# Kernel tuning notes

Measured on AMD Instinct MI355X. Metric: run time of the kernel, lower is better.

## Reference

```python
import jax, jax.numpy as jnp
import numpy as np

B, C, H, W = 4, 512, 64, 64
D = 512  # model_dim


def setup_inputs() -> dict:
    key = jax.random.key(0)
    ks = jax.random.split(key, 9)
    s = 0.02
    return {
        "q": jax.random.normal(ks[0], (B, C, H, W), dtype=jnp.float32),
        "Wq": jax.random.normal(ks[1], (D, C), dtype=jnp.float32) * s,
        "bq": jax.random.normal(ks[2], (D,), dtype=jnp.float32) * s,
        "Wk": jax.random.normal(ks[3], (D, C), dtype=jnp.float32) * s,
        "bk": jax.random.normal(ks[4], (D,), dtype=jnp.float32) * s,
        "Wv": jax.random.normal(ks[5], (D, C), dtype=jnp.float32) * s,
        "bv": jax.random.normal(ks[6], (D,), dtype=jnp.float32) * s,
        "Wo": jax.random.normal(ks[7], (C, D), dtype=jnp.float32) * s,
        "bo": jax.random.normal(ks[8], (C,), dtype=jnp.float32) * s,
    }


def reference(q, Wq, bq, Wk, bk, Wv, bv, Wo, bo):
    b, c, h, w = q.shape
    # 1x1 conv == per-pixel linear over channels; tokens s = h*w
    x = q.reshape(b, c, h * w)                      # (b, c, s)
    Q = jnp.einsum('bcs,dc->bsd', x, Wq) + bq       # (b, s, D)
    K = jnp.einsum('bcs,dc->bsd', x, Wk) + bk
    V = jnp.einsum('bcs,dc->bsd', x, Wv) + bv
    # ScaleAttend: scale = q.shape[-1]^-0.5 = model_dim^-0.5 (heads not split)
    scale = jnp.asarray(Q.shape[-1], Q.dtype) ** -0.5
    sim = jnp.einsum('bsd,btd->bst', Q, K) * scale  # (b, s, s)
    attn = jax.nn.softmax(sim, axis=-1)
    o = jnp.einsum('bst,btd->bsd', attn, V)         # (b, s, D)
    # to_out 1x1 conv: D -> C
    y = jnp.einsum('bsd,cd->bsc', o, Wo) + bo       # (b, s, C)
    return y.transpose(0, 2, 1).reshape(b, c, h, w)
```

## Files before the change

kernel.cpp:

```cpp
#include <hip/hip_runtime.h>
#include <hip/hip_bf16.h>

typedef __hip_bfloat16 bf16;
typedef __attribute__((ext_vector_type(8))) short short8;
typedef __attribute__((ext_vector_type(4))) float floatx4;
typedef __attribute__((ext_vector_type(4))) short shortx4;

static constexpr int BATCH = 4;
static constexpr int CH    = 512;
static constexpr int SEQ   = 4096;
static constexpr int DM    = 512;

__device__ __forceinline__ void gload16(const void* g, void* l) {
  __builtin_amdgcn_global_load_lds(
      (const __attribute__((address_space(1))) unsigned int*)g,
      (__attribute__((address_space(3))) unsigned int*)l,
      16, 0, 0);
}

__global__ __launch_bounds__(256) void cvt_weights(
    const float* __restrict__ w0, const float* __restrict__ w1,
    const float* __restrict__ w2, const float* __restrict__ w3,
    bf16* __restrict__ out) {
  const float* src = (blockIdx.y == 0) ? w0 : (blockIdx.y == 1) ? w1
                   : (blockIdx.y == 2) ? w2 : w3;
  int idx = blockIdx.x * 256 + threadIdx.x;
  out[(long)blockIdx.y * (DM * CH) + idx] = __float2bfloat16(src[idx]);
}

__global__ __launch_bounds__(256) void transpose_cvt(
    const float* __restrict__ x, bf16* __restrict__ xT) {
  __shared__ float tile[64][65];
  const int s0 = blockIdx.x * 64, c0 = blockIdx.y * 64;
  const float* xb = x + (long)blockIdx.z * CH * SEQ;
  bf16* xTb = xT + (long)blockIdx.z * SEQ * CH;
  const int t = threadIdx.x;
  const int sl = t & 63, cq = t >> 6;
  #pragma unroll
  for (int i = 0; i < 16; ++i) {
    int cl = cq * 16 + i;
    tile[cl][sl] = xb[(long)(c0 + cl) * SEQ + s0 + sl];
  }
  __syncthreads();
  const int cl2 = t & 63, sq = t >> 6;
  #pragma unroll
  for (int i = 0; i < 16; ++i) {
    int sl2 = sq * 16 + i;
    xTb[(long)(s0 + sl2) * CH + c0 + cl2] = __float2bfloat16(tile[cl2][sl2]);
  }
}

__global__ __launch_bounds__(512, 2) void gemm_qk(
    const bf16* __restrict__ A, long sAz,
    const bf16* __restrict__ B, long sBz,
    bf16* __restrict__ C, long sCz,
    float scale, int K, int ldc) {
  __shared__ __align__(16) bf16 As[2][256 * 64];
  __shared__ __align__(16) bf16 Bs[2][256 * 64];

  int id = blockIdx.x + gridDim.x * (blockIdx.y + gridDim.y * blockIdx.z);
  int nwg = gridDim.x * gridDim.y * gridDim.z;
  int sid = ((nwg & 7) == 0) ? ((id & 7) * (nwg >> 3) + (id >> 3)) : id;
  const int bx = sid % gridDim.x;
  const int by = (sid / gridDim.x) % gridDim.y;
  const int bz = sid / (gridDim.x * gridDim.y);

  const int tid = threadIdx.x;
  const long lK = K;
  const bf16* Ab = A + (long)bz * sAz + (long)by * 256 * lK;
  const bf16* Bb = B + (long)bz * sBz + (long)bx * 256 * lK;

  const int w = tid >> 6, lane = tid & 63;
  const int wr = w >> 2, wc = w & 3;
  const int l16 = lane & 15, quad = lane >> 4;

  const int srow = tid >> 3;
  const int sp = tid & 7;
  const int slog = (sp ^ (srow & 7)) << 3;

  const int pA0 = (quad ^ (l16 & 7)) << 3;
  const int pA1 = pA0 ^ 32;

  auto stage_half = [&](const bf16* Gb, bf16* Lb, int kt, int h) {
    #pragma unroll
    for (int r = 0; r < 2; ++r) {
      const int row = h * 128 + r * 64 + srow;
      gload16(Gb + (long)kt * 64 + (long)row * lK + slog,
              (char*)Lb + row * 128 + sp * 16);
    }
  };

  floatx4 acc[8][4];
  #pragma unroll
  for (int m = 0; m < 8; ++m)
    #pragma unroll
    for (int n = 0; n < 4; ++n) acc[m][n] = (floatx4)(0.0f);

  const int nk = K >> 6;
  stage_half(Ab, &As[0][0], 0, 0); stage_half(Bb, &Bs[0][0], 0, 0);
  stage_half(Ab, &As[0][0], 0, 1); stage_half(Bb, &Bs[0][0], 0, 1);
  if (nk > 1) { stage_half(Ab, &As[1][0], 1, 0); stage_half(Bb, &Bs[1][0], 1, 0); }
  asm volatile("s_waitcnt vmcnt(4)" ::: "memory");
  __builtin_amdgcn_s_barrier();

  for (int tt = 0; tt < nk; tt += 2) {
    #pragma unroll
    for (int u = 0; u < 2; ++u) {
      const bf16* __restrict__ Al = &As[u][0];
      const bf16* __restrict__ Bl = &Bs[u][0];
      short8 a[2][4], b[2][2][2];
      #pragma unroll
      for (int p = 0; p < 4; ++p) {
        const int rm = p >> 1, cn = p & 1;
        if (cn == 0) {
          #pragma unroll
          for (int kc = 0; kc < 2; ++kc)
            #pragma unroll
            for (int i = 0; i < 4; ++i)
              a[kc][i] = *(const short8*)(
                  Al + (rm * 128 + wr * 64 + i * 16 + l16) * 64
                     + (kc ? pA1 : pA0));
        }
        if (rm == 0) {
          #pragma unroll
          for (int kc = 0; kc < 2; ++kc)
            #pragma unroll
            for (int j = 0; j < 2; ++j)
              b[kc][cn][j] = *(const short8*)(
                  Bl + (cn * 128 + wc * 32 + j * 16 + l16) * 64
                     + (kc ? pA1 : pA0));
        }
        {
          const int g = u * 4 + p;
          const int stile = tt + 1 + ((g + 2) >> 2);
          if (stile < nk) {
            const int sh = (p < 2) ? 1 : 0;
            if (p & 1) stage_half(Bb, &Bs[stile & 1][0], stile, sh);
            else       stage_half(Ab, &As[stile & 1][0], stile, sh);
          }
        }
        __builtin_amdgcn_sched_barrier(0);
        __builtin_amdgcn_s_barrier();
        asm volatile("s_waitcnt lgkmcnt(0)" ::: "memory");
        __builtin_amdgcn_sched_barrier(0);
        __builtin_amdgcn_s_setprio(1);
        #pragma unroll
        for (int kc = 0; kc < 2; ++kc)
          #pragma unroll
          for (int i = 0; i < 4; ++i)
            #pragma unroll
            for (int j = 0; j < 2; ++j)
              acc[rm * 4 + i][cn * 2 + j] =
                  __builtin_amdgcn_mfma_f32_16x16x32_bf16(
                      a[kc][i], b[kc][cn][j], acc[rm * 4 + i][cn * 2 + j],
                      0, 0, 0);
        __builtin_amdgcn_s_setprio(0);
        if (p == 3) {
          if (u == 0) {
            if (tt + 2 < nk) asm volatile("s_waitcnt vmcnt(4)" ::: "memory");
            else             asm volatile("s_waitcnt vmcnt(0)" ::: "memory");
          } else {
            if (tt + 2 < nk) asm volatile("s_waitcnt vmcnt(4)" ::: "memory");
          }
        }
        __builtin_amdgcn_s_barrier();
      }
    }
  }

  bf16* Cb = C + (long)bz * sCz;
  #pragma unroll
  for (int rm = 0; rm < 2; ++rm)
    #pragma unroll
    for (int i = 0; i < 4; ++i) {
      const int row = by * 256 + rm * 128 + wr * 64 + i * 16 + quad * 4;
      #pragma unroll
      for (int cn = 0; cn < 2; ++cn)
        #pragma unroll
        for (int j = 0; j < 2; ++j) {
          const int col = bx * 256 + cn * 128 + wc * 32 + j * 16 + l16;
          floatx4 v = acc[rm * 4 + i][cn * 2 + j];
          #pragma unroll
          for (int r = 0; r < 4; ++r)
            Cb[(long)(row + r) * ldc + col] = __float2bfloat16(v[r] * scale);
        }
    }
}

template <int MODE>
__global__ __launch_bounds__(512, 2) void gemm_bn128(
    const bf16* __restrict__ A, long sAz,
    const bf16* __restrict__ B, long sBz,
    void* __restrict__ Cv, long sCz,
    const float* __restrict__ bias, float scale,
    int K, int ldc) {
  __shared__ __align__(16) bf16 As[3][256 * 64];
  __shared__ __align__(16) bf16 Bs[3][128 * 64];

  int id = blockIdx.x + gridDim.x * (blockIdx.y + gridDim.y * blockIdx.z);
  int nwg = gridDim.x * gridDim.y * gridDim.z;
  int sid = ((nwg & 7) == 0) ? ((id & 7) * (nwg >> 3) + (id >> 3)) : id;
  const int bx = sid % gridDim.x;
  const int by = (sid / gridDim.x) % gridDim.y;
  const int bz = sid / (gridDim.x * gridDim.y);

  const int tid = threadIdx.x;
  const long lK = K;
  const bf16* Ab = A + (long)bz * sAz + (long)by * 256 * lK;
  const bf16* Bb = B + (long)bz * sBz + (long)bx * 128 * lK;

  const int w = tid >> 6, lane = tid & 63;
  const int wr = w >> 1, wc = w & 1;
  const int l16 = lane & 15, quad = lane >> 4;

  const int srow = tid >> 3;
  const int sp = tid & 7;
  const int slog = (sp ^ (srow & 7)) << 3;

  const int pA0 = (quad ^ (l16 & 7)) << 3;
  const int pA1 = pA0 ^ 32;

  auto stageA = [&](int buf, int kt) {
    const bf16* s = Ab + (long)kt * 64 + (long)srow * lK + slog;
    char* d = (char*)(&As[buf][0]) + tid * 16;
    #pragma unroll
    for (int r = 0; r < 4; ++r)
      gload16(s + (long)(r * 64) * lK, d + r * 8192);
  };
  auto stageB = [&](int buf, int kt) {
    const bf16* s = Bb + (long)kt * 64 + (long)srow * lK + slog;
    char* d = (char*)(&Bs[buf][0]) + tid * 16;
    #pragma unroll
    for (int r = 0; r < 2; ++r)
      gload16(s + (long)(r * 64) * lK, d + r * 8192);
  };

  floatx4 acc[4][4];
  #pragma unroll
  for (int m = 0; m < 4; ++m)
    #pragma unroll
    for (int n = 0; n < 4; ++n) acc[m][n] = (floatx4)(0.0f);

  const int nk = K >> 6;
  stageA(0, 0); stageB(0, 0);
  stageA(1, 1); stageB(1, 1);
  asm volatile("s_waitcnt vmcnt(6)" ::: "memory");
  __builtin_amdgcn_s_barrier();

  int bcur = 0, bstage = 2;
  for (int t = 0; t < nk; ++t) {
    const bf16* __restrict__ Al = &As[bcur][0];
    const bf16* __restrict__ Bl = &Bs[bcur][0];
    const bool more = (t + 2 < nk);
    #pragma unroll
    for (int kc = 0; kc < 2; ++kc) {
      const int poff = kc ? pA1 : pA0;
      short8 a[4], b[4];
      #pragma unroll
      for (int i = 0; i < 4; ++i)
        a[i] = *(const short8*)(Al + (wr * 64 + i * 16 + l16) * 64 + poff);
      #pragma unroll
      for (int j = 0; j < 4; ++j)
        b[j] = *(const short8*)(Bl + (wc * 64 + j * 16 + l16) * 64 + poff);
      if (more) {
        if (kc == 0) stageA(bstage, t + 2);
        else         stageB(bstage, t + 2);
      }
      __builtin_amdgcn_s_barrier();
      __builtin_amdgcn_s_setprio(1);
      #pragma unroll
      for (int i = 0; i < 4; ++i)
        #pragma unroll
        for (int j = 0; j < 4; ++j)
          acc[i][j] = __builtin_amdgcn_mfma_f32_16x16x32_bf16(
              a[i], b[j], acc[i][j], 0, 0, 0);
      __builtin_amdgcn_s_setprio(0);
      if (kc == 1) {
        if (more)            asm volatile("s_waitcnt vmcnt(6)" ::: "memory");
        else if (t + 1 < nk) asm volatile("s_waitcnt vmcnt(0)" ::: "memory");
      }
      __builtin_amdgcn_s_barrier();
    }
    bcur = (bcur == 2) ? 0 : bcur + 1;
    bstage = (bstage == 2) ? 0 : bstage + 1;
  }

  const int rbase = by * 256 + wr * 64 + quad * 4;
  const int cbase = bx * 128 + wc * 64 + l16;
  #pragma unroll
  for (int m = 0; m < 4; ++m) {
    const int row = rbase + m * 16;
    #pragma unroll
    for (int n = 0; n < 4; ++n) {
      const int col = cbase + n * 16;
      floatx4 v = acc[m][n];
      if constexpr (MODE == 0) {
        bf16* C = (bf16*)Cv + (long)bz * sCz;
        const float bb = bias[col];
        #pragma unroll
        for (int r = 0; r < 4; ++r)
          C[(long)(row + r) * ldc + col] = __float2bfloat16(v[r] + bb);
      } else if constexpr (MODE == 1) {
        bf16* C = (bf16*)Cv + (long)bz * sCz;
        const float bb = bias[col];
        alignas(8) bf16 tmp[4];
        #pragma unroll
        for (int r = 0; r < 4; ++r) tmp[r] = __float2bfloat16(v[r] + bb);
        *(shortx4*)(C + (long)col * ldc + row) = *(const shortx4*)tmp;
      } else if constexpr (MODE == 2) {
        bf16* C = (bf16*)Cv + (long)bz * sCz;
        #pragma unroll
        for (int r = 0; r < 4; ++r)
          C[(long)(row + r) * ldc + col] = __float2bfloat16(v[r] * scale);
      } else {
        float* C = (float*)Cv + (long)bz * sCz;
        const float bb = bias[col];
        floatx4 o_;
        #pragma unroll
        for (int r = 0; r < 4; ++r) o_[r] = v[r] + bb;
        *(floatx4*)(C + (long)col * ldc + row) = o_;
      }
    }
  }
}

__global__ __launch_bounds__(256) void softmax_rows(bf16* __restrict__ sim) {
  bf16* p = sim + (long)blockIdx.y * ((long)SEQ * SEQ) + (long)blockIdx.x * SEQ;
  uint4* p4 = (uint4*)p;
  const int t = threadIdx.x;
  union U { uint4 u; ushort h[8]; } d[2];
  d[0].u = p4[t];
  d[1].u = p4[t + 256];
  float v[16];
  float mx = -3.0e38f;
  #pragma unroll
  for (int i = 0; i < 16; ++i) {
    v[i] = __uint_as_float(((unsigned)d[i >> 3].h[i & 7]) << 16);
    mx = fmaxf(mx, v[i]);
  }
  #pragma unroll
  for (int o = 32; o > 0; o >>= 1) mx = fmaxf(mx, __shfl_xor(mx, o));
  __shared__ float redmax[4], redsum[4];
  if ((t & 63) == 0) redmax[t >> 6] = mx;
  __syncthreads();
  mx = fmaxf(fmaxf(redmax[0], redmax[1]), fmaxf(redmax[2], redmax[3]));
  float sum = 0.f;
  #pragma unroll
  for (int i = 0; i < 16; ++i) {
    v[i] = __expf(v[i] - mx);
    sum += v[i];
  }
  #pragma unroll
  for (int o = 32; o > 0; o >>= 1) sum += __shfl_xor(sum, o);
  if ((t & 63) == 0) redsum[t >> 6] = sum;
  __syncthreads();
  sum = redsum[0] + redsum[1] + redsum[2] + redsum[3];
  const float inv = 1.0f / sum;
  union Hb { __hip_bfloat16 h; ushort u; };
  #pragma unroll
  for (int i = 0; i < 16; ++i) {
    Hb hb;
    hb.h = __float2bfloat16(v[i] * inv);
    d[i >> 3].h[i & 7] = hb.u;
  }
  p4[t] = d[0].u;
  p4[t + 256] = d[1].u;
}

extern "C" void kernel_launch(void* const* d_in, const int* in_sizes, int n_in,
                              void* d_out, int out_size, void* d_ws,
                              size_t ws_size, hipStream_t stream) {
  const float* q  = (const float*)d_in[0];
  const float* Wq = (const float*)d_in[1];
  const float* bq = (const float*)d_in[2];
  const float* Wk = (const float*)d_in[3];
  const float* bk = (const float*)d_in[4];
  const float* Wv = (const float*)d_in[5];
  const float* bv = (const float*)d_in[6];
  const float* Wo = (const float*)d_in[7];
  const float* bo = (const float*)d_in[8];
  float* out = (float*)d_out;

  bf16* ws = (bf16*)d_ws;
  const long WSZ = (long)DM * CH;
  const long XSZ = (long)SEQ * CH;
  const long SSZ = (long)SEQ * SEQ;
  bf16* Wqb = ws;
  bf16* Wkb = Wqb + WSZ;
  bf16* Wvb = Wqb + 2 * WSZ;
  bf16* Wob = Wqb + 3 * WSZ;
  bf16* xT  = Wqb + 4 * WSZ;
  bf16* Qb  = xT + BATCH * XSZ;
  bf16* Kb  = Qb + BATCH * XSZ;
  bf16* Vt  = Kb + BATCH * XSZ;
  bf16* Ob  = Vt + BATCH * XSZ;
  bf16* Sim = Ob + BATCH * XSZ;

  cvt_weights<<<dim3(WSZ / 256, 4), 256, 0, stream>>>(Wq, Wk, Wv, Wo, ws);
  transpose_cvt<<<dim3(SEQ / 64, CH / 64, BATCH), 256, 0, stream>>>(q, xT);

  gemm_bn128<0><<<dim3(4, 16, BATCH), 512, 0, stream>>>(
      xT, XSZ, Wqb, 0, Qb, XSZ, bq, 1.f, CH, DM);
  gemm_bn128<0><<<dim3(4, 16, BATCH), 512, 0, stream>>>(
      xT, XSZ, Wkb, 0, Kb, XSZ, bk, 1.f, CH, DM);
  gemm_bn128<1><<<dim3(4, 16, BATCH), 512, 0, stream>>>(
      xT, XSZ, Wvb, 0, Vt, XSZ, bv, 1.f, CH, SEQ);
  gemm_qk<<<dim3(16, 16, BATCH), 512, 0, stream>>>(
      Qb, XSZ, Kb, XSZ, Sim, SSZ, 0.04419417382415922f, CH, SEQ);
  softmax_rows<<<dim3(SEQ, BATCH), 256, 0, stream>>>(Sim);
  gemm_bn128<2><<<dim3(4, 16, BATCH), 512, 0, stream>>>(
      Sim, SSZ, Vt, XSZ, Ob, XSZ, nullptr, 1.0f, SEQ, DM);
  gemm_bn128<4><<<dim3(4, 16, BATCH), 512, 0, stream>>>(
      Ob, XSZ, Wob, 0, out, XSZ, bo, 1.f, DM, SEQ);
}
```

Before: 362.8 us.

## Fuse softmax into the P·V GEMM with online row statistics

Replaces the separate softmax kernel and the Sim×V GEMM with one kernel. Each block first scans its 64 rows of Sim to compute the running max and sum, then streams Sim again, applying exp(x - max) while staging tiles into LDS, multiplies by V with MFMA, and scales by 1/sum at the end. This removes the softmax read-modify-write pass over the 4096x4096 score matrix and one launch. In exchange Sim is read twice, and the grid drops to 256 blocks of 64 rows that each cover the full 512-wide output, with a global-load-latency-bound first pass, so occupancy and parallelism may suffer.

```diff
diff --git a/kernel.cpp b/kernel.cpp
--- a/kernel.cpp
+++ b/kernel.cpp
@@ -187,6 +187,141 @@
     }
 }
 
+__global__ __launch_bounds__(512, 2) void fused_smpv(
+    const bf16* __restrict__ Sim, const bf16* __restrict__ Vt,
+    bf16* __restrict__ Ob) {
+  __shared__ __align__(16) bf16 Apv[2][64 * 64];
+  __shared__ __align__(16) bf16 Bpv[2][512 * 64];
+  __shared__ float rl_lds[64];
+
+  const int id = blockIdx.x + (blockIdx.y << 6);
+  const int bz = (id >> 1) & 3;
+  const int by = ((id >> 3) << 1) | (id & 1);
+
+  const int tid = threadIdx.x;
+  const bf16* Simb = Sim + (long)bz * ((long)SEQ * SEQ) + (long)(by * 64) * SEQ;
+  const bf16* Vb   = Vt  + (long)bz * ((long)SEQ * CH);
+  bf16* Obb        = Ob  + (long)bz * ((long)SEQ * CH) + (long)(by * 64) * CH;
+
+  const int srow = tid >> 3;
+  const int sp = tid & 7;
+  const int slog = (sp ^ (srow & 7)) << 3;
+  const int aswz = (sp ^ (srow & 7)) << 4;
+
+  float m = -3.0e38f, l = 0.f;
+  {
+    const uint4* pr = (const uint4*)(Simb + (long)srow * SEQ) + sp;
+    for (int c = 0; c < 64; ++c) {
+      uint4 u = pr[c * 8];
+      const ushort* h = (const ushort*)&u;
+      float v[8];
+      float vm = -3.0e38f;
+      #pragma unroll
+      for (int k2 = 0; k2 < 8; ++k2) {
+        v[k2] = __uint_as_float(((unsigned)h[k2]) << 16);
+        vm = fmaxf(vm, v[k2]);
+      }
+      if (vm > m) { l *= __expf(m - vm); m = vm; }
+      #pragma unroll
+      for (int k2 = 0; k2 < 8; ++k2) l += __expf(v[k2] - m);
+    }
+    #pragma unroll
+    for (int o = 1; o < 8; o <<= 1) {
+      float m2 = __shfl_xor(m, o), l2 = __shfl_xor(l, o);
+      float nm = fmaxf(m, m2);
+      l = l * __expf(m - nm) + l2 * __expf(m2 - nm);
+      m = nm;
+    }
+    if (sp == 0) rl_lds[srow] = 1.0f / l;
+  }
+
+  const int w = tid >> 6, lane = tid & 63;
+  const int l16 = lane & 15, quad = lane >> 4;
+  const int pA0 = (quad ^ (l16 & 7)) << 3;
+  const int pA1 = pA0 ^ 32;
+
+  auto stageB8 = [&](int buf, int kt) {
+    const bf16* s = Vb + (long)srow * SEQ + kt * 64 + slog;
+    char* d = (char*)(&Bpv[buf][0]) + tid * 16;
+    #pragma unroll
+    for (int r = 0; r < 8; ++r)
+      gload16(s + (long)(r * 64) * SEQ, d + r * 8192);
+  };
+  auto writeA = [&](int buf, uint4 u) {
+    const ushort* h = (const ushort*)&u;
+    union { uint4 u4; ushort hh[8]; } pk;
+    #pragma unroll
+    for (int k2 = 0; k2 < 8; ++k2) {
+      float f = __uint_as_float(((unsigned)h[k2]) << 16);
+      __hip_bfloat16 pb = __float2bfloat16(__expf(f - m));
+      pk.hh[k2] = *(const ushort*)&pb;
+    }
+    *(uint4*)((char*)(&Apv[buf][0]) + srow * 128 + aswz) = pk.u4;
+  };
+
+  {
+    uint4 ua = *(const uint4*)(Simb + (long)srow * SEQ + sp * 8);
+    stageB8(0, 0);
+    writeA(0, ua);
+  }
+  __syncthreads();
+
+  floatx4 acc[4][4];
+  #pragma unroll
+  for (int i = 0; i < 4; ++i)
+    #pragma unroll
+    for (int j = 0; j < 4; ++j) acc[i][j] = (floatx4)(0.0f);
+
+  const int nk = SEQ >> 6;
+  for (int t = 0; t < nk; ++t) {
+    const int cur = t & 1, nxt = cur ^ 1;
+    const bool more = (t + 1 < nk);
+    uint4 un;
+    if (more) {
+      un = *(const uint4*)(Simb + (long)srow * SEQ + (t + 1) * 64 + sp * 8);
+      stageB8(nxt, t + 1);
+    }
+    short8 a[2][4], b[2][4];
+    #pragma unroll
+    for (int kc = 0; kc < 2; ++kc) {
+      const int poff = kc ? pA1 : pA0;
+      #pragma unroll
+      for (int i = 0; i < 4; ++i)
+        a[kc][i] = *(const short8*)(&Apv[cur][0] + (i * 16 + l16) * 64 + poff);
+      #pragma unroll
+      for (int j = 0; j < 4; ++j)
+        b[kc][j] = *(const short8*)(&Bpv[cur][0]
+                                    + (w * 64 + j * 16 + l16) * 64 + poff);
+    }
+    __builtin_amdgcn_s_setprio(1);
+    #pragma unroll
+    for (int kc = 0; kc < 2; ++kc)
+      #pragma unroll
+      for (int i = 0; i < 4; ++i)
+        #pragma unroll
+        for (int j = 0; j < 4; ++j)
+          acc[i][j] = __builtin_amdgcn_mfma_f32_16x16x32_bf16(
+              a[kc][i], b[kc][j], acc[i][j], 0, 0, 0);
+    __builtin_amdgcn_s_setprio(0);
+    if (more) writeA(nxt, un);
+    __syncthreads();
+  }
+
+  #pragma unroll
+  for (int i = 0; i < 4; ++i) {
+    #pragma unroll
+    for (int j = 0; j < 4; ++j) {
+      floatx4 v = acc[i][j];
+      const int col = w * 64 + j * 16 + l16;
+      #pragma unroll
+      for (int r = 0; r < 4; ++r) {
+        const int row = i * 16 + quad * 4 + r;
+        Obb[(long)row * CH + col] = __float2bfloat16(v[r] * rl_lds[row]);
+      }
+    }
+  }
+}
+
 template <int MODE>
 __global__ __launch_bounds__(512, 2) void gemm_bn128(
     const bf16* __restrict__ A, long sAz,
@@ -307,11 +442,6 @@
         #pragma unroll
         for (int r = 0; r < 4; ++r) tmp[r] = __float2bfloat16(v[r] + bb);
         *(shortx4*)(C + (long)col * ldc + row) = *(const shortx4*)tmp;
-      } else if constexpr (MODE == 2) {
-        bf16* C = (bf16*)Cv + (long)bz * sCz;
-        #pragma unroll
-        for (int r = 0; r < 4; ++r)
-          C[(long)(row + r) * ldc + col] = __float2bfloat16(v[r] * scale);
       } else {
         float* C = (float*)Cv + (long)bz * sCz;
         const float bb = bias[col];
@@ -322,49 +452,6 @@
       }
     }
   }
-}
-
-__global__ __launch_bounds__(256) void softmax_rows(bf16* __restrict__ sim) {
-  bf16* p = sim + (long)blockIdx.y * ((long)SEQ * SEQ) + (long)blockIdx.x * SEQ;
-  uint4* p4 = (uint4*)p;
-  const int t = threadIdx.x;
-  union U { uint4 u; ushort h[8]; } d[2];
-  d[0].u = p4[t];
-  d[1].u = p4[t + 256];
-  float v[16];
-  float mx = -3.0e38f;
-  #pragma unroll
-  for (int i = 0; i < 16; ++i) {
-    v[i] = __uint_as_float(((unsigned)d[i >> 3].h[i & 7]) << 16);
-    mx = fmaxf(mx, v[i]);
-  }
-  #pragma unroll
-  for (int o = 32; o > 0; o >>= 1) mx = fmaxf(mx, __shfl_xor(mx, o));
-  __shared__ float redmax[4], redsum[4];
-  if ((t & 63) == 0) redmax[t >> 6] = mx;
-  __syncthreads();
-  mx = fmaxf(fmaxf(redmax[0], redmax[1]), fmaxf(redmax[2], redmax[3]));
-  float sum = 0.f;
-  #pragma unroll
-  for (int i = 0; i < 16; ++i) {
-    v[i] = __expf(v[i] - mx);
-    sum += v[i];
-  }
-  #pragma unroll
-  for (int o = 32; o > 0; o >>= 1) sum += __shfl_xor(sum, o);
-  if ((t & 63) == 0) redsum[t >> 6] = sum;
-  __syncthreads();
-  sum = redsum[0] + redsum[1] + redsum[2] + redsum[3];
-  const float inv = 1.0f / sum;
-  union Hb { __hip_bfloat16 h; ushort u; };
-  #pragma unroll
-  for (int i = 0; i < 16; ++i) {
-    Hb hb;
-    hb.h = __float2bfloat16(v[i] * inv);
-    d[i >> 3].h[i & 7] = hb.u;
-  }
-  p4[t] = d[0].u;
-  p4[t + 256] = d[1].u;
 }
 
 extern "C" void kernel_launch(void* const* d_in, const int* in_sizes, int n_in,
@@ -407,9 +494,7 @@
       xT, XSZ, Wvb, 0, Vt, XSZ, bv, 1.f, CH, SEQ);
   gemm_qk<<<dim3(16, 16, BATCH), 512, 0, stream>>>(
       Qb, XSZ, Kb, XSZ, Sim, SSZ, 0.04419417382415922f, CH, SEQ);
-  softmax_rows<<<dim3(SEQ, BATCH), 256, 0, stream>>>(Sim);
-  gemm_bn128<2><<<dim3(4, 16, BATCH), 512, 0, stream>>>(
-      Sim, SSZ, Vt, XSZ, Ob, XSZ, nullptr, 1.0f, SEQ, DM);
+  fused_smpv<<<dim3(64, 4), 512, 0, stream>>>(Sim, Vt, Ob);
   gemm_bn128<4><<<dim3(4, 16, BATCH), 512, 0, stream>>>(
       Ob, XSZ, Wob, 0, out, XSZ, bo, 1.f, DM, SEQ);
 }
```

After: 378.9 us. 4.4% more time.
